# Performance work log

Measured on AMD Instinct MI355X. Metric: run time of the kernel, lower is better.

Reference implementation:

```python
import jax, jax.numpy as jnp
import numpy as np

K = 3
KK = K * K


def _offset_mask_conv(x, ow, ob):
    # Conv2d(C_in, 3*KK, k=3, stride=1, pad=1) in NCHW/OIHW
    y = jax.lax.conv_general_dilated(
        x, ow, window_strides=(1, 1), padding=((1, 1), (1, 1)),
        dimension_numbers=('NCHW', 'OIHW', 'NCHW'))
    return y + ob[None, :, None, None]


def _bilinear(xb, gy, gx):
    # xb: [C,H,W]; gy,gx: [KK,H,W] pixel coords (align_corners=True => pixel==unnormalized)
    # padding_mode='zeros': out-of-range taps contribute 0.
    C, H, W = xb.shape
    x0f = jnp.floor(gx); y0f = jnp.floor(gy)
    x0 = x0f.astype(jnp.int32); y0 = y0f.astype(jnp.int32)
    x1 = x0 + 1; y1 = y0 + 1
    wx1 = gx - x0f; wy1 = gy - y0f
    wx0 = 1.0 - wx1; wy0 = 1.0 - wy1

    def gather(yi, xi):
        valid = (yi >= 0) & (yi < H) & (xi >= 0) & (xi < W)
        yc = jnp.clip(yi, 0, H - 1)
        xc = jnp.clip(xi, 0, W - 1)
        v = xb[:, yc, xc]  # [C,KK,H,W]
        return v * valid[None].astype(xb.dtype)

    return (gather(y0, x0) * (wy0 * wx0)[None]
            + gather(y0, x1) * (wy0 * wx1)[None]
            + gather(y1, x0) * (wy1 * wx0)[None]
            + gather(y1, x1) * (wy1 * wx1)[None])  # [C,KK,H,W]


def setup_inputs() -> dict:
    key = jax.random.key(0)
    k1, k2, k3, k4 = jax.random.split(key, 4)
    B, C, Cout, H, W = 8, 64, 64, 128, 128
    x = jax.random.normal(k1, (B, C, H, W), dtype=jnp.float32)
    # offset/mask conv params (small, so offsets stay in a realistic range)
    ow = jax.random.normal(k2, (3 * KK, C, K, K), dtype=jnp.float32) * 0.01
    ob = jnp.zeros((3 * KK,), dtype=jnp.float32)
    # main conv weight (kaiming-ish scale) and bias
    w = jax.random.normal(k3, (Cout, C, K, K), dtype=jnp.float32) * (1.0 / np.sqrt(C * KK))
    b = jax.random.normal(k4, (Cout,), dtype=jnp.float32) * 0.01
    return {"x": x, "ow": ow, "ob": ob, "w": w, "b": b}


def reference(x, ow, ob, w, b):
    B, C, H, W = x.shape
    om = _offset_mask_conv(x, ow, ob)            # [B, 3*KK, H, W]
    off_x = om[:, :KK]                           # o1 -> x-offset
    off_y = om[:, KK:2 * KK]                     # o2 -> y-offset
    mask = jax.nn.sigmoid(om[:, 2 * KK:])        # [B,KK,H,W]

    gh, gw = jnp.meshgrid(jnp.arange(H, dtype=x.dtype), jnp.arange(W, dtype=x.dtype), indexing='ij')
    d = jnp.arange(-(K // 2), K // 2 + 1, dtype=x.dtype)
    kh, kw = jnp.meshgrid(d, d, indexing='ij')
    dh = kh.reshape(-1)                          # [KK] row-major (dh,dw) order matches weight[...,i,j]
    dw = kw.reshape(-1)

    gx = gw[None, None] + dw[None, :, None, None] + off_x   # [B,KK,H,W]
    gy = gh[None, None] + dh[None, :, None, None] + off_y

    sampled = jax.vmap(_bilinear)(x, gy, gx)     # [B,C,KK,H,W]
    sampled = sampled * mask[:, None]            # modulation

    wflat = w.reshape(w.shape[0], w.shape[1], KK)  # [Cout,C,KK]
    out = jnp.einsum('bckhw,ock->bohw', sampled, wflat) + b[None, :, None, None]
    return out
```

## Files before the change

kernel.cpp:

```cpp
#include <hip/hip_runtime.h>

#define B 8
#define C 64
#define H 128
#define W 128
#define HW (H * W)
#define OC 27
#define KK 9
#define COUT 64
#define KDIM 576
#define LDSROW 1152
#define NPIX 16
#define NPAIR (NPIX * KK)

typedef __attribute__((ext_vector_type(8))) short s16x8;
typedef __attribute__((ext_vector_type(4))) float f32x4;

__device__ inline ushort f2bf(float f) {
    union { float f; unsigned u; } uv;
    uv.f = f;
    unsigned r = uv.u + 0x7FFF + ((uv.u >> 16) & 1);
    return (ushort)(r >> 16);
}
__device__ inline float bf2f(ushort u) {
    return __uint_as_float((unsigned)u << 16);
}

__global__ __launch_bounds__(256) void k_transpose_x(const float* __restrict__ x,
                                                     ushort* __restrict__ xTb) {
    __shared__ float lds[64][65];
    int b = blockIdx.x >> 8;
    int tile = blockIdx.x & 255;
    int hw0 = tile * 64;
    int lane = threadIdx.x & 63;
    int cg = threadIdx.x >> 6;
#pragma unroll
    for (int r = 0; r < 16; ++r) {
        int c = cg * 16 + r;
        lds[c][lane] = x[(size_t)(b * C + c) * HW + hw0 + lane];
    }
    __syncthreads();
#pragma unroll
    for (int r = 0; r < 16; ++r) {
        int hwl = cg * 16 + r;
        xTb[(size_t)(b * HW + hw0 + hwl) * C + lane] = f2bf(lds[lane][hwl]);
    }
}

__global__ __launch_bounds__(256) void k_prep_w(const float* __restrict__ w,
                                                ushort* __restrict__ wB) {
    int idx = blockIdx.x * 256 + threadIdx.x;
    if (idx >= COUT * KDIM) return;
    int o = idx / KDIM;
    int Kx = idx % KDIM;
    int k = Kx >> 6;
    int c = Kx & 63;
    wB[idx] = f2bf(w[(size_t)(o * C + c) * KK + k]);
}

__global__ __launch_bounds__(256) void k_prep_aw(const float* __restrict__ ow,
                                                 ushort* __restrict__ awB) {
    int idx = blockIdx.x * 256 + threadIdx.x;
    if (idx >= 32 * KDIM) return;
    int o = idx / KDIM;
    int Kx = idx % KDIM;
    int tap = Kx >> 6;
    int c = Kx & 63;
    float v = (o < OC) ? ow[((size_t)o * C + c) * KK + tap] : 0.0f;
    awB[idx] = f2bf(v);
}

__global__ __launch_bounds__(256) void k_om(const ushort* __restrict__ xTb,
                                            const ushort* __restrict__ awB,
                                            const float* __restrict__ ob,
                                            float* __restrict__ om) {
    __shared__ __align__(16) char xwin[3 * 66 * 128];
    int tid = threadIdx.x;
    int lane = tid & 63;
    int wv = tid >> 6;
    int blk = blockIdx.x;
    int b = blk >> 8;
    int h = (blk >> 1) & 127;
    int w0 = (blk & 1) * 64;

    const ushort* xb = xTb + (size_t)b * (HW * C);
    int ch2 = tid & 31;
#pragma unroll
    for (int it = 0; it < 25; ++it) {
        int pi = it * 8 + (tid >> 5);
        if (pi < 198) {
            int row = pi / 66;
            int col = pi - row * 66;
            int y = h - 1 + row;
            int xc = w0 - 1 + col;
            unsigned v = 0;
            if ((unsigned)y < H && (unsigned)xc < W)
                v = *(const unsigned*)(xb + ((size_t)(y * W + xc) << 6) + ch2 * 2);
            int byte = (pi * 128 + ch2 * 4) ^ ((col & 7) << 4);
            *(unsigned*)(xwin + byte) = v;
        }
    }
    __syncthreads();

    f32x4 acc0 = {0.f, 0.f, 0.f, 0.f};
    f32x4 acc1 = {0.f, 0.f, 0.f, 0.f};
    int pixl = lane & 15;
    int q = lane >> 4;
    int base_col = wv * 16 + pixl;
    const ushort* a0 = awB + (size_t)pixl * KDIM + q * 8;
    const ushort* a1 = awB + (size_t)(16 + pixl) * KDIM + q * 8;
#pragma unroll
    for (int s = 0; s < 18; ++s) {
        int tap = s >> 1;
        int row = tap / 3;
        int cs = tap - row * 3;
        int col = base_col + cs;
        int c0b = ((s & 1) * 32 + q * 8) * 2;
        int byte = (((row * 66 + col) << 7) + c0b) ^ ((col & 7) << 4);
        s16x8 bfrag = *(const s16x8*)(xwin + byte);
        s16x8 af0 = *(const s16x8*)(a0 + s * 32);
        s16x8 af1 = *(const s16x8*)(a1 + s * 32);
        acc0 = __builtin_amdgcn_mfma_f32_16x16x32_bf16(af0, bfrag, acc0, 0, 0, 0);
        acc1 = __builtin_amdgcn_mfma_f32_16x16x32_bf16(af1, bfrag, acc1, 0, 0, 0);
    }

    int pix = wv * 16 + pixl;
#pragma unroll
    for (int j = 0; j < 4; ++j) {
        int oc = q * 4 + j;
        om[(((size_t)b * OC + oc) * H + h) * W + w0 + pix] = acc0[j] + ob[oc];
        int oc1 = 16 + q * 4 + j;
        if (oc1 < OC)
            om[(((size_t)b * OC + oc1) * H + h) * W + w0 + pix] = acc1[j] + ob[oc1];
    }
}

__global__ __launch_bounds__(256, 6) void k_main(const ushort* __restrict__ xTb,
                                                 const float* __restrict__ om,
                                                 const ushort* __restrict__ wB,
                                                 const float* __restrict__ bias,
                                                 float* __restrict__ out) {
    __shared__ __align__(16) char smem[NPIX * LDSROW];
    __shared__ float4 meta_w[NPAIR];
    __shared__ int2 meta_o[NPAIR];

    int tid = threadIdx.x;
    int lane = tid & 63;
    int wv = tid >> 6;
    int pb = blockIdx.x * NPIX;
    int b = pb >> 14;
    int rem = pb & (HW - 1);
    int h = rem >> 7;
    int w0 = rem & (W - 1);

    if (tid < NPAIR) {
        int k = tid >> 4;
        int p = tid & 15;
        int dh = k / 3 - 1;
        int dw = k % 3 - 1;
        const float* o0 = om + ((size_t)b * OC) * HW + h * W + w0 + p;
        float offx = o0[(size_t)k * HW];
        float offy = o0[(size_t)(KK + k) * HW];
        float mlog = o0[(size_t)(2 * KK + k) * HW];
        float mask = 1.0f / (1.0f + __expf(-mlog));
        float gx = (float)(w0 + p + dw) + offx;
        float gy = (float)(h + dh) + offy;
        float x0f = floorf(gx), y0f = floorf(gy);
        int x0 = (int)x0f, y0 = (int)y0f;
        int x1 = x0 + 1, y1 = y0 + 1;
        float wx1 = gx - x0f, wy1 = gy - y0f;
        float wx0 = 1.0f - wx1, wy0 = 1.0f - wy1;
        float rw0 = ((unsigned)y0 < H) ? wy0 * mask : 0.0f;
        float rw1 = ((unsigned)y1 < H) ? wy1 * mask : 0.0f;
        int y0c = min(max(y0, 0), H - 1), y1c = min(max(y1, 0), H - 1);
        int colbase = min(max(x0, 0), W - 2);
        float cw0 = 0.0f, cw1 = 0.0f;
        if ((unsigned)x0 < W) { if (x0 == colbase) cw0 += wx0; else cw1 += wx0; }
        if ((unsigned)x1 < W) { if (x1 == colbase) cw0 += wx1; else cw1 += wx1; }
        meta_w[tid] = make_float4(rw0 * cw0, rw0 * cw1, rw1 * cw0, rw1 * cw1);
        meta_o[tid] = make_int2((y0c * W + colbase) * (C * 2),
                                (y1c * W + colbase) * (C * 2));
    }
    __syncthreads();

    const char* xbase = (const char*)(xTb + (size_t)b * (HW * C));
    bool lo_half = lane < 32;
#pragma unroll
    for (int pp = 0; pp < 4; ++pp) {
        int p = wv * 4 + pp;
        unsigned d0[KK], d1[KK];
        float wa[KK], wb[KK];
#pragma unroll
        for (int k = 0; k < KK; ++k) {
            int pair = k * 16 + p;
            float4 mw = meta_w[pair];
            int2 mo = meta_o[pair];
            wa[k] = lo_half ? mw.x : mw.y;
            wb[k] = lo_half ? mw.z : mw.w;
            d0[k] = *(const unsigned*)(xbase + mo.x + lane * 4);
            d1[k] = *(const unsigned*)(xbase + mo.y + lane * 4);
        }
        int vlds = p * LDSROW + (((lane & 31) * 4) ^ ((p & 7) << 4));
#pragma unroll
        for (int k = 0; k < KK; ++k) {
            float a0 = __uint_as_float(d0[k] << 16);
            float a1 = __uint_as_float(d0[k] & 0xFFFF0000u);
            float b0 = __uint_as_float(d1[k] << 16);
            float b1 = __uint_as_float(d1[k] & 0xFFFF0000u);
            float p0 = a0 * wa[k] + b0 * wb[k];
            float p1 = a1 * wa[k] + b1 * wb[k];
            float q0 = __shfl_xor(p0, 32, 64);
            float q1 = __shfl_xor(p1, 32, 64);
            float s0 = p0 + q0, s1 = p1 + q1;
            unsigned pk;
            asm("v_cvt_pk_bf16_f32 %0, %1, %2" : "=v"(pk) : "v"(s0), "v"(s1));
            if (lane < 32) *(unsigned*)(smem + vlds + k * 128) = pk;
        }
    }
    __syncthreads();

    f32x4 acc;
#pragma unroll
    for (int j = 0; j < 4; ++j) acc[j] = bias[wv * 16 + (lane >> 4) * 4 + j];

    int pix = lane & 15;
    const ushort* wrow = wB + (size_t)(wv * 16 + pix) * KDIM + (lane >> 4) * 8;
#pragma unroll
    for (int s = 0; s < 18; ++s) {
        int kbyte = s * 64 + (lane >> 4) * 16;
        int byte = (pix * LDSROW + kbyte) ^ ((pix & 7) << 4);
        s16x8 bfrag = *(const s16x8*)(smem + byte);
        s16x8 afrag = *(const s16x8*)(wrow + s * 32);
        acc = __builtin_amdgcn_mfma_f32_16x16x32_bf16(afrag, bfrag, acc, 0, 0, 0);
    }

    float* obase = out + ((size_t)(b * COUT + wv * 16 + (lane >> 4) * 4) * HW) + h * W + w0;
#pragma unroll
    for (int j = 0; j < 4; ++j) obase[(size_t)j * HW + pix] = acc[j];
}

extern "C" void kernel_launch(void* const* d_in, const int* in_sizes, int n_in,
                              void* d_out, int out_size, void* d_ws, size_t ws_size,
                              hipStream_t stream) {
    const float* x = (const float*)d_in[0];
    const float* ow = (const float*)d_in[1];
    const float* ob = (const float*)d_in[2];
    const float* w = (const float*)d_in[3];
    const float* bias = (const float*)d_in[4];
    float* out = (float*)d_out;

    float* om = (float*)d_ws;
    ushort* xTb = (ushort*)(om + (size_t)B * OC * HW);
    ushort* wB = xTb + (size_t)B * HW * C;
    ushort* awB = wB + (size_t)COUT * KDIM;

    hipLaunchKernelGGL(k_transpose_x, dim3(B * 256), dim3(256), 0, stream, x, xTb);
    hipLaunchKernelGGL(k_prep_w, dim3((COUT * KDIM + 255) / 256), dim3(256), 0,
                       stream, w, wB);
    hipLaunchKernelGGL(k_prep_aw, dim3((32 * KDIM + 255) / 256), dim3(256), 0,
                       stream, ow, awB);
    hipLaunchKernelGGL(k_om, dim3(B * H * 2), dim3(256), 0, stream, xTb, awB, ob, om);
    hipLaunchKernelGGL(k_main, dim3(B * HW / NPIX), dim3(256), 0, stream,
                       xTb, om, wB, bias, out);
}
```

Before: 170.4 us.

## Fuse bilinear metadata computation into offset conv and remap block order

The offset/mask conv kernel now stages its outputs in LDS and computes per-pixel bilinear weights and gather offsets directly, writing them to global memory in pixel-major order. The main kernel then loads precomputed metadata instead of reading strided om channels and recomputing sigmoid and floor math. Block indices in three kernels are swizzled across the batch, presumably to spread work across XCDs or L2. The gather loop is no longer unrolled, has a scheduling barrier, and uses a launch bound of 5. In exchange, the intermediate buffer grows from 27 floats to 9×24 bytes per pixel, adding global traffic.

```diff
diff --git a/kernel.cpp b/kernel.cpp
--- a/kernel.cpp
+++ b/kernel.cpp
@@ -29,8 +29,10 @@
 __global__ __launch_bounds__(256) void k_transpose_x(const float* __restrict__ x,
                                                      ushort* __restrict__ xTb) {
     __shared__ float lds[64][65];
-    int b = blockIdx.x >> 8;
-    int tile = blockIdx.x & 255;
+    int j = blockIdx.x;
+    int vb = (j & 7) * 256 + (j >> 3);
+    int b = vb >> 8;
+    int tile = vb & 255;
     int hw0 = tile * 64;
     int lane = threadIdx.x & 63;
     int cg = threadIdx.x >> 6;
@@ -73,15 +75,17 @@
 __global__ __launch_bounds__(256) void k_om(const ushort* __restrict__ xTb,
                                             const ushort* __restrict__ awB,
                                             const float* __restrict__ ob,
-                                            float* __restrict__ om) {
+                                            float4* __restrict__ gW,
+                                            int2* __restrict__ gO) {
     __shared__ __align__(16) char xwin[3 * 66 * 128];
     int tid = threadIdx.x;
     int lane = tid & 63;
     int wv = tid >> 6;
-    int blk = blockIdx.x;
-    int b = blk >> 8;
-    int h = (blk >> 1) & 127;
-    int w0 = (blk & 1) * 64;
+    int j = blockIdx.x;
+    int vb = (j & 7) * 256 + (j >> 3);
+    int b = vb >> 8;
+    int h = (vb >> 1) & 127;
+    int w0 = (vb & 1) * 64;
 
     const ushort* xb = xTb + (size_t)b * (HW * C);
     int ch2 = tid & 31;
@@ -124,46 +128,34 @@
         acc1 = __builtin_amdgcn_mfma_f32_16x16x32_bf16(af1, bfrag, acc1, 0, 0, 0);
     }
 
-    int pix = wv * 16 + pixl;
-#pragma unroll
-    for (int j = 0; j < 4; ++j) {
-        int oc = q * 4 + j;
-        om[(((size_t)b * OC + oc) * H + h) * W + w0 + pix] = acc0[j] + ob[oc];
-        int oc1 = 16 + q * 4 + j;
-        if (oc1 < OC)
-            om[(((size_t)b * OC + oc1) * H + h) * W + w0 + pix] = acc1[j] + ob[oc1];
-    }
-}
-
-__global__ __launch_bounds__(256, 6) void k_main(const ushort* __restrict__ xTb,
-                                                 const float* __restrict__ om,
-                                                 const ushort* __restrict__ wB,
-                                                 const float* __restrict__ bias,
-                                                 float* __restrict__ out) {
-    __shared__ __align__(16) char smem[NPIX * LDSROW];
-    __shared__ float4 meta_w[NPAIR];
-    __shared__ int2 meta_o[NPAIR];
-
-    int tid = threadIdx.x;
-    int lane = tid & 63;
-    int wv = tid >> 6;
-    int pb = blockIdx.x * NPIX;
-    int b = pb >> 14;
-    int rem = pb & (HW - 1);
-    int h = rem >> 7;
-    int w0 = rem & (W - 1);
-
-    if (tid < NPAIR) {
-        int k = tid >> 4;
-        int p = tid & 15;
+    __syncthreads();
+    float* omt = (float*)xwin;
+    {
+        int pix = wv * 16 + pixl;
+#pragma unroll
+        for (int jj = 0; jj < 4; ++jj) {
+            int oc = q * 4 + jj;
+            omt[pix * 29 + oc] = acc0[jj] + ob[oc];
+        }
+#pragma unroll
+        for (int jj = 0; jj < 4; ++jj) {
+            int oc1 = 16 + q * 4 + jj;
+            if (oc1 < OC) omt[pix * 29 + oc1] = acc1[jj] + ob[oc1];
+        }
+    }
+    __syncthreads();
+
+    size_t base9 = ((size_t)b * HW + h * W + w0) * KK;
+    for (int t = tid; t < 64 * KK; t += 256) {
+        int pix = t / 9;
+        int k = t - pix * 9;
+        float offx = omt[pix * 29 + k];
+        float offy = omt[pix * 29 + 9 + k];
+        float mlog = omt[pix * 29 + 18 + k];
         int dh = k / 3 - 1;
         int dw = k % 3 - 1;
-        const float* o0 = om + ((size_t)b * OC) * HW + h * W + w0 + p;
-        float offx = o0[(size_t)k * HW];
-        float offy = o0[(size_t)(KK + k) * HW];
-        float mlog = o0[(size_t)(2 * KK + k) * HW];
         float mask = 1.0f / (1.0f + __expf(-mlog));
-        float gx = (float)(w0 + p + dw) + offx;
+        float gx = (float)(w0 + pix + dw) + offx;
         float gy = (float)(h + dh) + offy;
         float x0f = floorf(gx), y0f = floorf(gy);
         int x0 = (int)x0f, y0 = (int)y0f;
@@ -177,38 +169,68 @@
         float cw0 = 0.0f, cw1 = 0.0f;
         if ((unsigned)x0 < W) { if (x0 == colbase) cw0 += wx0; else cw1 += wx0; }
         if ((unsigned)x1 < W) { if (x1 == colbase) cw0 += wx1; else cw1 += wx1; }
-        meta_w[tid] = make_float4(rw0 * cw0, rw0 * cw1, rw1 * cw0, rw1 * cw1);
-        meta_o[tid] = make_int2((y0c * W + colbase) * (C * 2),
-                                (y1c * W + colbase) * (C * 2));
-    }
+        gW[base9 + t] = make_float4(rw0 * cw0, rw0 * cw1, rw1 * cw0, rw1 * cw1);
+        gO[base9 + t] = make_int2((y0c * W + colbase) * (C * 2),
+                                  (y1c * W + colbase) * (C * 2));
+    }
+}
+
+__global__ __launch_bounds__(256, 5) void k_main(const ushort* __restrict__ xTb,
+                                                 const float4* __restrict__ gW,
+                                                 const int2* __restrict__ gO,
+                                                 const ushort* __restrict__ wB,
+                                                 const float* __restrict__ bias,
+                                                 float* __restrict__ out) {
+    __shared__ __align__(16) char smem[NPIX * LDSROW];
+    __shared__ float4 mw_lds[NPAIR];
+    __shared__ int2 mo_lds[NPAIR];
+
+    int tid = threadIdx.x;
+    int lane = tid & 63;
+    int wv = tid >> 6;
+    int jb = blockIdx.x;
+    int vb = (jb & 7) * 1024 + (jb >> 3);
+    int pb = vb * NPIX;
+    int b = pb >> 14;
+    int rem = pb & (HW - 1);
+    int h = rem >> 7;
+    int w0 = rem & (W - 1);
+
+    size_t base9 = ((size_t)b * HW + rem) * KK;
+    if (tid < NPAIR) mw_lds[tid] = gW[base9 + tid];
+    if (tid < NPAIR) mo_lds[tid] = gO[base9 + tid];
     __syncthreads();
 
     const char* xbase = (const char*)(xTb + (size_t)b * (HW * C));
     bool lo_half = lane < 32;
-#pragma unroll
+#pragma unroll 1
     for (int pp = 0; pp < 4; ++pp) {
         int p = wv * 4 + pp;
+        float4 mwv[KK];
+        int2 mov[KK];
+#pragma unroll
+        for (int k = 0; k < KK; ++k) {
+            mwv[k] = mw_lds[p * 9 + k];
+            mov[k] = mo_lds[p * 9 + k];
+        }
         unsigned d0[KK], d1[KK];
-        float wa[KK], wb[KK];
 #pragma unroll
         for (int k = 0; k < KK; ++k) {
-            int pair = k * 16 + p;
-            float4 mw = meta_w[pair];
-            int2 mo = meta_o[pair];
-            wa[k] = lo_half ? mw.x : mw.y;
-            wb[k] = lo_half ? mw.z : mw.w;
-            d0[k] = *(const unsigned*)(xbase + mo.x + lane * 4);
-            d1[k] = *(const unsigned*)(xbase + mo.y + lane * 4);
-        }
+            d0[k] = *(const unsigned*)(xbase + mov[k].x + lane * 4);
+            d1[k] = *(const unsigned*)(xbase + mov[k].y + lane * 4);
+        }
+        __builtin_amdgcn_sched_barrier(0);
         int vlds = p * LDSROW + (((lane & 31) * 4) ^ ((p & 7) << 4));
 #pragma unroll
         for (int k = 0; k < KK; ++k) {
+            float wa = lo_half ? mwv[k].x : mwv[k].y;
+            float wb_ = lo_half ? mwv[k].z : mwv[k].w;
             float a0 = __uint_as_float(d0[k] << 16);
             float a1 = __uint_as_float(d0[k] & 0xFFFF0000u);
             float b0 = __uint_as_float(d1[k] << 16);
             float b1 = __uint_as_float(d1[k] & 0xFFFF0000u);
-            float p0 = a0 * wa[k] + b0 * wb[k];
-            float p1 = a1 * wa[k] + b1 * wb[k];
+            float p0 = a0 * wa + b0 * wb_;
+            float p1 = a1 * wa + b1 * wb_;
             float q0 = __shfl_xor(p0, 32, 64);
             float q1 = __shfl_xor(p1, 32, 64);
             float s0 = p0 + q0, s1 = p1 + q1;
@@ -249,8 +271,9 @@
     const float* bias = (const float*)d_in[4];
     float* out = (float*)d_out;
 
-    float* om = (float*)d_ws;
-    ushort* xTb = (ushort*)(om + (size_t)B * OC * HW);
+    float4* gW = (float4*)d_ws;
+    int2* gO = (int2*)(gW + (size_t)B * HW * KK);
+    ushort* xTb = (ushort*)(gO + (size_t)B * HW * KK);
     ushort* wB = xTb + (size_t)B * HW * C;
     ushort* awB = wB + (size_t)COUT * KDIM;
 
@@ -259,7 +282,7 @@
                        stream, w, wB);
     hipLaunchKernelGGL(k_prep_aw, dim3((32 * KDIM + 255) / 256), dim3(256), 0,
                        stream, ow, awB);
-    hipLaunchKernelGGL(k_om, dim3(B * H * 2), dim3(256), 0, stream, xTb, awB, ob, om);
+    hipLaunchKernelGGL(k_om, dim3(B * H * 2), dim3(256), 0, stream, xTb, awB, ob, gW, gO);
     hipLaunchKernelGGL(k_main, dim3(B * HW / NPIX), dim3(256), 0, stream,
-                       xTb, om, wB, bias, out);
-}
+                       xTb, gW, gO, wB, bias, out);
+}
```

After: 162.8 us. -4.5%, faster.
